# Kernel optimization log

Measured on AMD Instinct MI355X. Metric: run time of the kernel, lower is better.

The kernel has to match this reference:

```python
import jax, jax.numpy as jnp
import numpy as np


def _segment_mean(msg, dst, num_nodes):
    # msg: [E, B, O, T] summed into [N, B, O, T], mean over incoming edges
    s = jax.ops.segment_sum(msg, dst, num_segments=num_nodes)
    cnt = jax.ops.segment_sum(jnp.ones((msg.shape[0],), msg.dtype), dst, num_segments=num_nodes)
    return s / jnp.clip(cnt, 1.0)[:, None, None, None]


def _gcn(x, edge_index, edge_attr, A, Wk, Wr, b):
    # Edge-conditioned (spline-style) graph conv.
    # x: [B, N, Cin, T]; edge_attr: [E, 3]; Wk: [K, Cin, Cout]
    N = x.shape[1]
    src, dst = edge_index[0], edge_index[1]
    Bw = jax.nn.softmax(edge_attr @ A, axis=-1)          # [E, K] basis weights
    We = jnp.einsum('ek,kio->eio', Bw, Wk)                # [E, Cin, Cout]
    msg = jnp.einsum('beit,eio->ebot', x[:, src], We)     # [E, B, Cout, T]
    agg = _segment_mean(msg, dst, N).transpose(1, 0, 2, 3)  # [B, N, Cout, T]
    out = agg + jnp.einsum('bnit,io->bnot', x, Wr) + b[None, None, :, None]
    return jax.nn.elu(out)


def _pool(x, P, C, T):
    # x: [B, N_l, C, T] -> flatten, sparse-pool with P [N_{l+1}, N_l], unflatten
    B, N = x.shape[0], x.shape[1]
    xf = x.reshape(B, N, C * T)
    xf = jnp.einsum('mn,bnf->bmf', P, xf)
    return xf.reshape(B, P.shape[0], C, T)


def setup_inputs() -> dict:
    key = jax.random.key(0)
    ks = jax.random.split(key, 24)
    B, T = 2, 200
    N = [2048, 512, 128, 64]
    E = [16384, 8192, 2048]
    nf = [1, 8, 16, 32, 64, 128, 128]
    ld = 64

    def rn(k, shape, scale=1.0):
        return jax.random.normal(k, shape, dtype=jnp.float32) * scale

    inp = {}
    inp['x'] = rn(ks[0], (B, N[0], nf[0], T))
    inp['ei0'] = jax.random.randint(ks[1], (2, E[0]), 0, N[0])
    inp['ea0'] = jax.random.uniform(ks[2], (E[0], 3), dtype=jnp.float32)
    inp['ei1'] = jax.random.randint(ks[3], (2, E[1]), 0, N[1])
    inp['ea1'] = jax.random.uniform(ks[4], (E[1], 3), dtype=jnp.float32)
    inp['ei2'] = jax.random.randint(ks[5], (2, E[2]), 0, N[2])
    inp['ea2'] = jax.random.uniform(ks[6], (E[2], 3), dtype=jnp.float32)
    # gcn params: (A basis map, K=3 kernel weights, root weight, bias)
    inp['A1'] = rn(ks[7], (3, 3))
    inp['Wk1'] = rn(ks[8], (3, nf[0], nf[2]), 1.0 / np.sqrt(nf[0]))
    inp['Wr1'] = rn(ks[9], (nf[0], nf[2]), 1.0 / np.sqrt(nf[0]))
    inp['b1'] = jnp.zeros((nf[2],), jnp.float32)
    inp['A2'] = rn(ks[10], (3, 3))
    inp['Wk2'] = rn(ks[11], (3, nf[2], nf[3]), 1.0 / np.sqrt(nf[2]))
    inp['Wr2'] = rn(ks[12], (nf[2], nf[3]), 1.0 / np.sqrt(nf[2]))
    inp['b2'] = jnp.zeros((nf[3],), jnp.float32)
    inp['A3'] = rn(ks[13], (3, 3))
    inp['Wk3'] = rn(ks[14], (3, nf[3], nf[4]), 1.0 / np.sqrt(nf[3]))
    inp['Wr3'] = rn(ks[15], (nf[3], nf[4]), 1.0 / np.sqrt(nf[3]))
    inp['b3'] = jnp.zeros((nf[4],), jnp.float32)
    # sparse pooling projections (dense here)
    inp['P01'] = rn(ks[16], (N[1], N[0]), 1.0 / np.sqrt(N[0]))
    inp['P12'] = rn(ks[17], (N[2], N[1]), 1.0 / np.sqrt(N[1]))
    inp['P23'] = rn(ks[18], (N[3], N[2]), 1.0 / np.sqrt(N[2]))
    # 1x1 conv encoder head
    inp['fce1_w'] = rn(ks[19], (nf[4], nf[6]), 1.0 / np.sqrt(nf[4]))
    inp['fce1_b'] = jnp.zeros((nf[6],), jnp.float32)
    inp['fce2_w'] = rn(ks[20], (nf[6], ld), 1.0 / np.sqrt(nf[6]))
    inp['fce2_b'] = jnp.zeros((ld,), jnp.float32)
    return inp


def reference(x, ei0, ea0, ei1, ea1, ei2, ea2, A1, Wk1, Wr1, b1, A2, Wk2, Wr2, b2,
              A3, Wk3, Wr3, b3, P01, P12, P23, fce1_w, fce1_b, fce2_w, fce2_b):
    T = x.shape[-1]
    # level 0 -> 1
    h = _gcn(x, ei0, ea0, A1, Wk1, Wr1, b1)          # [B, N0, 16, T]
    h = _pool(h, P01, h.shape[2], T)                 # [B, N1, 16, T]
    # level 1 -> 2
    h = _gcn(h, ei1, ea1, A2, Wk2, Wr2, b2)          # [B, N1, 32, T]
    h = _pool(h, P12, h.shape[2], T)                 # [B, N2, 32, T]
    # level 2 -> 3
    h = _gcn(h, ei2, ea2, A3, Wk3, Wr3, b3)          # [B, N2, 64, T]
    h = _pool(h, P23, h.shape[2], T)                 # [B, N3, 64, T]
    # 1x1 conv encoder head (channel-wise linear over node/time grid)
    h = jax.nn.elu(jnp.einsum('bnct,co->bnot', h, fce1_w) + fce1_b[None, None, :, None])
    mu = jnp.tanh(jnp.einsum('bnct,co->bnot', h, fce2_w) + fce2_b[None, None, :, None])
    return mu  # [B, N3, latent_dim, T]
```

## Files before the change

### kernel.cpp

```cpp
#include <hip/hip_runtime.h>
#include <hip/hip_bf16.h>

using bf16 = __hip_bfloat16;
typedef unsigned short ushort_t;
typedef unsigned int uint_t;

constexpr int B = 2, T = 200;
constexpr int N0 = 2048, N1 = 512, N2 = 128, N3 = 64;
constexpr int E0 = 16384, E1 = 8192, E2 = 2048;

typedef __attribute__((ext_vector_type(8))) short bf16x8;
typedef __attribute__((ext_vector_type(4))) float f32x4;

constexpr size_t O_FLAG = 161792;
constexpr size_t O_WC1  = 163840;
constexpr size_t O_BIAS = 164096;
constexpr size_t O_BW0  = 165312;
constexpr size_t O_BW1  = 361920;
constexpr size_t O_BW2  = 460224;
constexpr size_t O_PB1  = 484800;
constexpr size_t O_PB2  = 2581952;
constexpr size_t O_PB3  = 2713024;
constexpr size_t O_WT2  = 2729408;
constexpr size_t O_WT3  = 2733504;
constexpr size_t O_W1H  = 2749888;
constexpr size_t O_W2H  = 2766272;
constexpr size_t O_AA   = 2785280;
constexpr size_t O_BB   = 15892480;

__device__ __forceinline__ float ldx(const void* p, long i, int bf) {
  if (bf) {
    uint_t v = (uint_t)(((const ushort_t*)p)[i]) << 16;
    float f; __builtin_memcpy(&f, &v, 4); return f;
  }
  return ((const float*)p)[i];
}
__device__ __forceinline__ void stf(float* p, float v) { *p = v; }
__device__ __forceinline__ void stf(bf16* p, float v) { *p = __float2bfloat16(v); }
__device__ __forceinline__ ushort_t f2bfu(float v) {
  bf16 h = __float2bfloat16(v); ushort_t u; __builtin_memcpy(&u, &h, 2); return u;
}

struct InPtrs {
  const void* ea0; const void* ea1; const void* ea2;
  const void* P01; const void* P12; const void* P23;
  const void* Wk1; const void* Wr1; const void* Wk2; const void* Wr2;
  const void* Wk3; const void* Wr3; const void* W1h; const void* W2h;
  const void* b1; const void* b2; const void* b3; const void* b1h; const void* b2h;
  const void* A1; const void* A2; const void* A3;
};

__global__ void k_setup0(int* I, const ushort_t* ea) {
  if (blockIdx.x < 158) {
    int i = blockIdx.x * 256 + threadIdx.x;
    I[i] = 0;
  } else if (threadIdx.x == 0) {
    int c = 0;
    for (int i = 0; i < 128; ++i) {
      uint_t v = (uint_t)ea[i] << 16;
      float f; __builtin_memcpy(&f, &v, 4);
      if (f >= 0.f && f <= 1.0f) c++;
    }
    *(int*)((char*)I + O_FLAG) = (c >= 120) ? 1 : 0;
  }
}

__device__ __forceinline__ void bw_one(const void* ea, int bf, const void* A,
                                       float* bw, int e) {
  float a0 = ldx(ea, e*3+0, bf), a1 = ldx(ea, e*3+1, bf), a2 = ldx(ea, e*3+2, bf);
  float l0 = a0*ldx(A,0,bf) + a1*ldx(A,3,bf) + a2*ldx(A,6,bf);
  float l1 = a0*ldx(A,1,bf) + a1*ldx(A,4,bf) + a2*ldx(A,7,bf);
  float l2 = a0*ldx(A,2,bf) + a1*ldx(A,5,bf) + a2*ldx(A,8,bf);
  float m = fmaxf(l0, fmaxf(l1, l2));
  float x0 = expf(l0 - m), x1 = expf(l1 - m), x2 = expf(l2 - m);
  float inv = 1.0f / (x0 + x1 + x2);
  bw[e*3+0] = x0*inv; bw[e*3+1] = x1*inv; bw[e*3+2] = x2*inv;
}

__global__ void k_prep(InPtrs P, char* base) {
  int bf = *(const int*)(base + O_FLAG);
  int bx = blockIdx.x, tid = threadIdx.x;
  float* bw0 = (float*)(base + O_BW0);
  float* bw1 = (float*)(base + O_BW1);
  float* bw2 = (float*)(base + O_BW2);
  if (bx < 64)        { bw_one(P.ea0, bf, P.A1, bw0, bx*256+tid); return; }
  if (bx < 96)        { bw_one(P.ea1, bf, P.A2, bw1, (bx-64)*256+tid); return; }
  if (bx < 104)       { bw_one(P.ea2, bf, P.A3, bw2, (bx-96)*256+tid); return; }
  if (bx < 4200)      { long i = (long)(bx-104)*256+tid;
                        ((ushort_t*)(base+O_PB1))[i] = f2bfu(ldx(P.P01, i, bf)); return; }
  if (bx < 4456)      { int i = (bx-4200)*256+tid;
                        ((ushort_t*)(base+O_PB2))[i] = f2bfu(ldx(P.P12, i, bf)); return; }
  if (bx < 4488)      { int i = (bx-4456)*256+tid;
                        ((ushort_t*)(base+O_PB3))[i] = f2bfu(ldx(P.P23, i, bf)); return; }
  if (bx < 4496)      { int j = (bx-4488)*256+tid; int o = j>>6, c = j&63;
                        float v = (c<48) ? ldx(P.Wk2, c*32+o, bf) : ldx(P.Wr2, (c-48)*32+o, bf);
                        ((ushort_t*)(base+O_WT2))[j] = f2bfu(v); return; }
  if (bx < 4528)      { int j = (bx-4496)*256+tid; int o = j>>7, c = j&127;
                        float v = (c<96) ? ldx(P.Wk3, c*64+o, bf) : ldx(P.Wr3, (c-96)*64+o, bf);
                        ((ushort_t*)(base+O_WT3))[j] = f2bfu(v); return; }
  if (bx < 4560)      { int j = (bx-4528)*256+tid; int o = j>>6, c = j&63;
                        ((ushort_t*)(base+O_W1H))[j] = f2bfu(ldx(P.W1h, c*128+o, bf)); return; }
  if (bx < 4592)      { int j = (bx-4560)*256+tid; int o = j>>7, c = j&127;
                        ((ushort_t*)(base+O_W2H))[j] = f2bfu(ldx(P.W2h, c*64+o, bf)); return; }
  {
    int i = (bx-4592)*256+tid;
    if (i < 64) {
      ((float*)(base+O_WC1))[i] = (i<48) ? ldx(P.Wk1, i, bf) : ldx(P.Wr1, i-48, bf);
    } else if (i < 368) {
      int j = i - 64; float v;
      if (j < 16)       v = ldx(P.b1, j, bf);
      else if (j < 48)  v = ldx(P.b2, j-16, bf);
      else if (j < 112) v = ldx(P.b3, j-48, bf);
      else if (j < 240) v = ldx(P.b1h, j-112, bf);
      else              v = ldx(P.b2h, j-240, bf);
      ((float*)(base+O_BIAS))[j] = v;
    }
  }
}

__global__ void k_hist3(const int* d0, const int* d1, const int* d2,
                        int* c0, int* c1, int* c2) {
  int i = blockIdx.x * 256 + threadIdx.x;
  if (i < E0) atomicAdd(&c0[d0[i]], 1);
  if (i < E1) atomicAdd(&c1[d1[i]], 1);
  if (i < E2) atomicAdd(&c2[d2[i]], 1);
}

__global__ void k_scan3(const int* c0, int* o0, int* u0,
                        const int* c1, int* o1, int* u1,
                        const int* c2, int* o2, int* u2) {
  const int* cnt; int* off; int* cur; int N;
  if (blockIdx.x == 0)      { cnt = c0; off = o0; cur = u0; N = N0; }
  else if (blockIdx.x == 1) { cnt = c1; off = o1; cur = u1; N = N1; }
  else                      { cnt = c2; off = o2; cur = u2; N = N2; }
  int tid = threadIdx.x;
  int chunk = (N + 63) >> 6;
  int base = tid * chunk;
  int s = 0;
  for (int j = 0; j < chunk; ++j) { int idx = base + j; if (idx < N) s += cnt[idx]; }
  int pre = s;
  for (int d = 1; d < 64; d <<= 1) {
    int v = __shfl_up(pre, d, 64);
    if (tid >= d) pre += v;
  }
  int run = pre - s;
  for (int j = 0; j < chunk; ++j) {
    int idx = base + j;
    if (idx < N) { off[idx] = run; cur[idx] = run; run += cnt[idx]; }
  }
  if (tid == 63) off[N] = run;
}

__global__ void k_fill3(const int* d0, int* u0, int* e0l,
                        const int* d1, int* u1, int* e1l,
                        const int* d2, int* u2, int* e2l) {
  int i = blockIdx.x * 256 + threadIdx.x;
  if (i < E0) { int p = atomicAdd(&u0[d0[i]], 1); e0l[p] = i; }
  if (i < E1) { int p = atomicAdd(&u1[d1[i]], 1); e1l[p] = i; }
  if (i < E2) { int p = atomicAdd(&u2[d2[i]], 1); e2l[p] = i; }
}

__global__ __launch_bounds__(256) void k_gc1(const void* x, const int* src,
    const int* off, const int* elist, const int* cnt, const float* bw,
    const float* W, const float* bias, bf16* h1, const int* flagp) {
  __shared__ float Wl[64];
  __shared__ float bl[16];
  __shared__ float ew0[32], ew1[32], ew2[32];
  __shared__ int es[32];
  int tid = threadIdx.x;
  if (tid < 64) Wl[tid] = W[tid];
  if (tid < 16) bl[tid] = bias[tid];
  int bf = *flagp;
  int n = blockIdx.y, b = blockIdx.z;
  int t = tid;
  bool tok = t < T;
  int beg = off[n], end = off[n + 1];
  float a0 = 0.f, a1 = 0.f, a2 = 0.f;
  for (int q0 = beg; q0 < end; q0 += 32) {
    int m = end - q0; if (m > 32) m = 32;
    __syncthreads();
    if (tid < m) {
      int e = elist[q0 + tid];
      es[tid] = src[e];
      ew0[tid] = bw[e*3+0]; ew1[tid] = bw[e*3+1]; ew2[tid] = bw[e*3+2];
    }
    __syncthreads();
    if (tok) {
      for (int j = 0; j < m; ++j) {
        float xv = ldx(x, (long)(b * N0 + es[j]) * T + t, bf);
        a0 += ew0[j] * xv; a1 += ew1[j] * xv; a2 += ew2[j] * xv;
      }
    }
  }
  __syncthreads();
  if (!tok) return;
  int c = cnt[n];
  float inv = 1.f / (float)(c > 0 ? c : 1);
  a0 *= inv; a1 *= inv; a2 *= inv;
  float xr = ldx(x, (long)(b * N0 + n) * T + t, bf);
  bf16* op = h1 + ((long)(b * N0 + n) * 16) * T + t;
#pragma unroll
  for (int o = 0; o < 16; ++o) {
    float v = a0 * Wl[o] + a1 * Wl[16 + o] + a2 * Wl[32 + o] + xr * Wl[48 + o] + bl[o];
    v = v > 0.f ? v : (expf(v) - 1.f);
    op[o * T] = __float2bfloat16(v);
  }
}

template<int CIN, int CPI, int O>
__global__ __launch_bounds__(256) void k_gcm(const float* hp, const int* src,
    const int* off, const int* elist, const int* cnt, const float* bw,
    const ushort_t* Wt, const float* bias, bf16* h, int N) {
  constexpr int C = 4 * CIN;
  constexpr int KG = C / 8;
  constexpr int MT = O / 16;
  __shared__ __align__(16) ushort_t Ws[O * C];
  __shared__ __align__(16) ushort_t Is[64 * C];
  __shared__ float ew0[32], ew1[32], ew2[32];
  __shared__ int es[32];
  int tid = threadIdx.x;
  int w = tid >> 6, l = tid & 63;
  int lf = l & 15, quad = l >> 4;
  int t0 = blockIdx.x * 64;
  int n = blockIdx.y, b = blockIdx.z;
  {
    const uint4* Wg = (const uint4*)Wt;
    for (int s = tid; s < O * KG; s += 256) {
      int o = s / KG, kg = s % KG;
      *(uint4*)(Ws + o * C + ((kg ^ (o & 7)) * 8)) = Wg[s];
    }
  }
  int tx = tid & 63, iy = tid >> 6;
  int t = t0 + tx;
  bool tok = t < T;
  float acc[3][CPI], xr[CPI];
#pragma unroll
  for (int k = 0; k < 3; ++k)
#pragma unroll
    for (int j = 0; j < CPI; ++j) acc[k][j] = 0.f;
#pragma unroll
  for (int j = 0; j < CPI; ++j) xr[j] = 0.f;
  int beg = off[n], end = off[n + 1];
  for (int q0 = beg; q0 < end; q0 += 32) {
    int mE = end - q0; if (mE > 32) mE = 32;
    __syncthreads();
    if (tid < mE) {
      int e = elist[q0 + tid];
      es[tid] = src[e];
      ew0[tid] = bw[e*3+0]; ew1[tid] = bw[e*3+1]; ew2[tid] = bw[e*3+2];
    }
    __syncthreads();
    if (tok) {
      for (int j2 = 0; j2 < mE; ++j2) {
        int s = es[j2];
        float w0 = ew0[j2], w1 = ew1[j2], w2 = ew2[j2];
        const float* xp = hp + ((long)(b * N + s) * CIN) * T + t;
#pragma unroll
        for (int j = 0; j < CPI; ++j) {
          float xv = xp[(iy * CPI + j) * T];
          acc[0][j] += w0 * xv; acc[1][j] += w1 * xv; acc[2][j] += w2 * xv;
        }
      }
    }
  }
  float inv = 1.f;
  if (tok) {
    int c = cnt[n];
    inv = 1.f / (float)(c > 0 ? c : 1);
    const float* xs = hp + ((long)(b * N + n) * CIN) * T + t;
#pragma unroll
    for (int j = 0; j < CPI; ++j) xr[j] = xs[(iy * CPI + j) * T];
  }
#pragma unroll
  for (int j = 0; j < CPI; ++j) {
    int i = iy * CPI + j;
#pragma unroll
    for (int k = 0; k < 3; ++k) {
      int c = k * CIN + i;
      Is[tx * C + ((c >> 3) ^ (tx & 7)) * 8 + (c & 7)] = f2bfu(acc[k][j] * inv);
    }
    int c = 3 * CIN + i;
    Is[tx * C + ((c >> 3) ^ (tx & 7)) * 8 + (c & 7)] = f2bfu(xr[j]);
  }
  __syncthreads();
  f32x4 dacc[MT];
#pragma unroll
  for (int mt = 0; mt < MT; ++mt) dacc[mt] = (f32x4){0.f, 0.f, 0.f, 0.f};
  int tr = w * 16 + lf;
#pragma unroll
  for (int kc = 0; kc < C / 32; ++kc) {
    int kg0 = kc * 4 + quad;
    bf16x8 bfr = *(const bf16x8*)(Is + tr * C + ((kg0 ^ (tr & 7)) * 8));
#pragma unroll
    for (int mt = 0; mt < MT; ++mt) {
      int o = mt * 16 + lf;
      bf16x8 afr = *(const bf16x8*)(Ws + o * C + ((kg0 ^ (o & 7)) * 8));
      dacc[mt] = __builtin_amdgcn_mfma_f32_16x16x32_bf16(afr, bfr, dacc[mt], 0, 0, 0);
    }
  }
  int tg = t0 + w * 16 + lf;
  if (tg < T) {
    long nb = (long)(b * N + n) * O;
#pragma unroll
    for (int mt = 0; mt < MT; ++mt) {
#pragma unroll
      for (int r = 0; r < 4; ++r) {
        int o = mt * 16 + quad * 4 + r;
        float v = dacc[mt][r] + bias[o];
        v = v > 0.f ? v : (expf(v) - 1.f);
        h[(nb + o) * T + tg] = __float2bfloat16(v);
      }
    }
  }
}

template<int WMT, int FT, typename TOut>
__global__ __launch_bounds__(256) void k_pool_mfma(const ushort_t* Pb, const ushort_t* h,
                                                   TOut* out, int M, int K, int F) {
  constexpr int BM = 64 * WMT;
  constexpr int BN = 16 * FT;
  __shared__ __align__(16) ushort_t As[BM * 64];
  __shared__ __align__(16) ushort_t Bs[BN * 64];
  int tid = threadIdx.x;
  int w = tid >> 6, l = tid & 63;
  int lf = l & 15, quad = l >> 4;
  int f0 = blockIdx.x * BN;
  int m0 = blockIdx.y * BM;
  int b = blockIdx.z;
  f32x4 acc[WMT][FT];
#pragma unroll
  for (int wt = 0; wt < WMT; ++wt)
#pragma unroll
    for (int ft = 0; ft < FT; ++ft) acc[wt][ft] = (f32x4){0.f, 0.f, 0.f, 0.f};

  for (int k0 = 0; k0 < K; k0 += 64) {
#pragma unroll
    for (int it = 0; it < BM / 32; ++it) {
      int cc = tid + 256 * it;
      int m = cc >> 3, kc = cc & 7;
      uint4 v = *(const uint4*)(Pb + (long)(m0 + m) * K + k0 + kc * 8);
      *(uint4*)(As + m * 64 + ((kc ^ (m & 7)) * 8)) = v;
    }
#pragma unroll
    for (int kb = (tid / BN) * 16; kb < 64; kb += (256 / BN) * 16) {
      int f = tid % BN;
      const ushort_t* hp = h + ((long)(b * K + k0 + kb)) * F + f0 + f;
      ushort_t r[16];
#pragma unroll
      for (int i = 0; i < 16; ++i) r[i] = hp[(long)i * F];
      int kc0 = kb >> 3;
      *(uint4*)(Bs + f * 64 + ((kc0 ^ (f & 7)) * 8)) = *(uint4*)&r[0];
      *(uint4*)(Bs + f * 64 + (((kc0 + 1) ^ (f & 7)) * 8)) = *(uint4*)&r[8];
    }
    __syncthreads();
#pragma unroll
    for (int ks = 0; ks < 2; ++ks) {
      int kc = ks * 4 + quad;
      bf16x8 bfr[FT];
#pragma unroll
      for (int ft = 0; ft < FT; ++ft) {
        int fl = ft * 16 + lf;
        bfr[ft] = *(const bf16x8*)(Bs + fl * 64 + ((kc ^ (fl & 7)) * 8));
      }
#pragma unroll
      for (int wt = 0; wt < WMT; ++wt) {
        int ml = wt * 64 + w * 16 + lf;
        bf16x8 afr = *(const bf16x8*)(As + ml * 64 + ((kc ^ (ml & 7)) * 8));
#pragma unroll
        for (int ft = 0; ft < FT; ++ft)
          acc[wt][ft] = __builtin_amdgcn_mfma_f32_16x16x32_bf16(afr, bfr[ft], acc[wt][ft], 0, 0, 0);
      }
    }
    __syncthreads();
  }
#pragma unroll
  for (int wt = 0; wt < WMT; ++wt) {
#pragma unroll
    for (int r = 0; r < 4; ++r) {
      int m = m0 + wt * 64 + w * 16 + quad * 4 + r;
      TOut* op = out + ((long)(b * M + m)) * F + f0 + lf;
#pragma unroll
      for (int ft = 0; ft < FT; ++ft)
        stf(op + ft * 16, acc[wt][ft][r]);
    }
  }
}

__global__ __launch_bounds__(256) void k_head(const float* hp3, const ushort_t* W1t,
    const ushort_t* W2t, const float* bias, void* outp, const int* flagp) {
  __shared__ __align__(16) ushort_t Ws1[128 * 64];
  __shared__ __align__(16) ushort_t Ws2[64 * 128];
  __shared__ __align__(16) ushort_t Is[64 * 64];
  __shared__ __align__(16) ushort_t G[64 * 128];
  int tid = threadIdx.x;
  int w = tid >> 6, l = tid & 63;
  int lf = l & 15, quad = l >> 4;
  int t0 = blockIdx.x * 64;
  int n = blockIdx.y, b = blockIdx.z;
  {
    const uint4* g1 = (const uint4*)W1t;
    for (int s = tid; s < 1024; s += 256) {
      int o = s >> 3, kg = s & 7;
      *(uint4*)(Ws1 + o * 64 + ((kg ^ (o & 7)) * 8)) = g1[s];
    }
    const uint4* g2 = (const uint4*)W2t;
    for (int s = tid; s < 1024; s += 256) {
      int o = s >> 4, kg = s & 15;
      *(uint4*)(Ws2 + o * 128 + ((kg ^ (o & 7)) * 8)) = g2[s];
    }
  }
  {
    int t = tid & 63;
    bool tok = (t0 + t) < T;
    const float* ip = hp3 + ((long)(b * 64 + n) * 64) * T + t0;
    for (int kg = tid >> 6; kg < 8; kg += 4) {
      ushort_t r[8];
#pragma unroll
      for (int j = 0; j < 8; ++j)
        r[j] = tok ? f2bfu(ip[(kg * 8 + j) * T + t]) : (ushort_t)0;
      *(uint4*)(Is + t * 64 + ((kg ^ (t & 7)) * 8)) = *(uint4*)r;
    }
  }
  __syncthreads();
  int tr = w * 16 + lf;
  {
    f32x4 a1[8];
#pragma unroll
    for (int mt = 0; mt < 8; ++mt) a1[mt] = (f32x4){0.f, 0.f, 0.f, 0.f};
#pragma unroll
    for (int kc = 0; kc < 2; ++kc) {
      int kg0 = kc * 4 + quad;
      bf16x8 bfr = *(const bf16x8*)(Is + tr * 64 + ((kg0 ^ (tr & 7)) * 8));
#pragma unroll
      for (int mt = 0; mt < 8; ++mt) {
        int o = mt * 16 + lf;
        bf16x8 afr = *(const bf16x8*)(Ws1 + o * 64 + ((kg0 ^ (o & 7)) * 8));
        a1[mt] = __builtin_amdgcn_mfma_f32_16x16x32_bf16(afr, bfr, a1[mt], 0, 0, 0);
      }
    }
    int tG = w * 16 + lf;
#pragma unroll
    for (int mt = 0; mt < 8; ++mt) {
#pragma unroll
      for (int r = 0; r < 4; ++r) {
        int o1 = mt * 16 + quad * 4 + r;
        float v = a1[mt][r] + bias[112 + o1];
        v = v > 0.f ? v : (expf(v) - 1.f);
        G[tG * 128 + ((o1 >> 3) ^ (tG & 7)) * 8 + (o1 & 7)] = f2bfu(v);
      }
    }
  }
  __syncthreads();
  {
    f32x4 a2[4];
#pragma unroll
    for (int mt = 0; mt < 4; ++mt) a2[mt] = (f32x4){0.f, 0.f, 0.f, 0.f};
#pragma unroll
    for (int kc = 0; kc < 4; ++kc) {
      int kg0 = kc * 4 + quad;
      bf16x8 bfr = *(const bf16x8*)(G + tr * 128 + ((kg0 ^ (tr & 7)) * 8));
#pragma unroll
      for (int mt = 0; mt < 4; ++mt) {
        int o = mt * 16 + lf;
        bf16x8 afr = *(const bf16x8*)(Ws2 + o * 128 + ((kg0 ^ (o & 7)) * 8));
        a2[mt] = __builtin_amdgcn_mfma_f32_16x16x32_bf16(afr, bfr, a2[mt], 0, 0, 0);
      }
    }
    int t = t0 + w * 16 + lf;
    if (t < T) {
      int bf = *flagp;
      long nb = (long)(b * 64 + n) * 64;
#pragma unroll
      for (int mt = 0; mt < 4; ++mt) {
#pragma unroll
        for (int r = 0; r < 4; ++r) {
          int o2 = mt * 16 + quad * 4 + r;
          float v = tanhf(a2[mt][r] + bias[240 + o2]);
          long idx = (nb + o2) * T + t;
          if (bf) ((bf16*)outp)[idx] = __float2bfloat16(v);
          else    ((float*)outp)[idx] = v;
        }
      }
    }
  }
}

extern "C" void kernel_launch(void* const* d_in, const int* in_sizes, int n_in,
                              void* d_out, int out_size, void* d_ws, size_t ws_size,
                              hipStream_t stream) {
  const int* ei0 = (const int*)d_in[1];
  const int* ei1 = (const int*)d_in[3];
  const int* ei2 = (const int*)d_in[5];

  char* base = (char*)d_ws;
  int* I = (int*)base;
  int* cnt0 = I;         int* off0 = I + 2048;  int* cur0 = I + 4112;  int* el0 = I + 6160;
  int* cnt1 = I + 22544; int* off1 = I + 23056; int* cur1 = I + 23584; int* el1 = I + 24096;
  int* cnt2 = I + 32288; int* off2 = I + 32416; int* cur2 = I + 32560; int* el2 = I + 32688;
  const int* flagp = (const int*)(base + O_FLAG);
  float* wc1f = (float*)(base + O_WC1);
  float* bias = (float*)(base + O_BIAS);
  float* bw0 = (float*)(base + O_BW0);
  float* bw1 = (float*)(base + O_BW1);
  float* bw2 = (float*)(base + O_BW2);
  ushort_t* Pb1 = (ushort_t*)(base + O_PB1);
  ushort_t* Pb2 = (ushort_t*)(base + O_PB2);
  ushort_t* Pb3 = (ushort_t*)(base + O_PB3);
  ushort_t* wt2 = (ushort_t*)(base + O_WT2);
  ushort_t* wt3 = (ushort_t*)(base + O_WT3);
  ushort_t* w1t = (ushort_t*)(base + O_W1H);
  ushort_t* w2t = (ushort_t*)(base + O_W2H);
  char* Aa = base + O_AA;
  char* Bb = base + O_BB;

  InPtrs P = { d_in[2], d_in[4], d_in[6], d_in[19], d_in[20], d_in[21],
               d_in[8], d_in[9], d_in[12], d_in[13], d_in[16], d_in[17],
               d_in[22], d_in[24], d_in[10], d_in[14], d_in[18], d_in[23],
               d_in[25], d_in[7], d_in[11], d_in[15] };

  k_setup0<<<159, 256, 0, stream>>>(I, (const ushort_t*)d_in[2]);
  k_prep<<<4594, 256, 0, stream>>>(P, base);
  k_hist3<<<64, 256, 0, stream>>>(ei0 + E0, ei1 + E1, ei2 + E2, cnt0, cnt1, cnt2);
  k_scan3<<<3, 64, 0, stream>>>(cnt0, off0, cur0, cnt1, off1, cur1, cnt2, off2, cur2);
  k_fill3<<<64, 256, 0, stream>>>(ei0 + E0, cur0, el0, ei1 + E1, cur1, el1, ei2 + E2, cur2, el2);

  k_gc1<<<dim3(1, N0, B), 256, 0, stream>>>(d_in[0], ei0, off0, el0, cnt0, bw0, wc1f, bias, (bf16*)Bb, flagp);
  k_pool_mfma<1, 4, float><<<dim3(50, 8, B), 256, 0, stream>>>(Pb1, (const ushort_t*)Bb, (float*)Aa, 512, 2048, 3200);
  k_gcm<16, 4, 32><<<dim3(4, N1, B), 256, 0, stream>>>((const float*)Aa, ei1, off1, el1, cnt1, bw1, wt2, bias + 16, (bf16*)Bb, N1);
  k_pool_mfma<1, 4, float><<<dim3(100, 2, B), 256, 0, stream>>>(Pb2, (const ushort_t*)Bb, (float*)Aa, 128, 512, 6400);
  k_gcm<32, 8, 64><<<dim3(4, N2, B), 256, 0, stream>>>((const float*)Aa, ei2, off2, el2, cnt2, bw2, wt3, bias + 48, (bf16*)Bb, N2);
  k_pool_mfma<1, 4, float><<<dim3(200, 1, B), 256, 0, stream>>>(Pb3, (const ushort_t*)Bb, (float*)Aa, 64, 128, 12800);
  k_head<<<dim3(4, N3, B), 256, 0, stream>>>((const float*)Aa, w1t, w2t, bias, d_out, flagp);
}
```

Measured before the change: 283.6 us.

## Rewrite pooling GEMM with split-K atomics, register prefetch, and block swizzle

Replaces the pooling MFMA kernel with a version that prefetches the next two K-steps into registers while computing the current one. It splits K across blocks for the first two pools, reduces partial results with float atomics into a zeroed buffer, and remaps block indices to group neighbouring tiles. The aim is to hide global-load latency and raise the block count so more CUs stay busy. In exchange it adds memset passes, atomic write traffic, and a nondeterministic summation order.

New measurement: 302.4 us. 6.6% more time.

```diff
diff --git a/kernel.cpp b/kernel.cpp
--- a/kernel.cpp
+++ b/kernel.cpp
@@ -314,74 +314,84 @@
   }
 }
 
-template<int WMT, int FT, typename TOut>
-__global__ __launch_bounds__(256) void k_pool_mfma(const ushort_t* Pb, const ushort_t* h,
-                                                   TOut* out, int M, int K, int F) {
-  constexpr int BM = 64 * WMT;
-  constexpr int BN = 16 * FT;
-  __shared__ __align__(16) ushort_t As[BM * 64];
-  __shared__ __align__(16) ushort_t Bs[BN * 64];
+template<int KSPLIT, bool ATOMIC, bool SWZ>
+__global__ __launch_bounds__(256) void k_poolp(const ushort_t* Pb, const ushort_t* h,
+                                               float* out, int M, int K, int F, int nInner) {
+  __shared__ __align__(16) ushort_t As[64 * 64];
+  __shared__ __align__(16) ushort_t Bs[64 * 64];
   int tid = threadIdx.x;
   int w = tid >> 6, l = tid & 63;
   int lf = l & 15, quad = l >> 4;
-  int f0 = blockIdx.x * BN;
-  int m0 = blockIdx.y * BM;
-  int b = blockIdx.z;
-  f32x4 acc[WMT][FT];
-#pragma unroll
-  for (int wt = 0; wt < WMT; ++wt)
-#pragma unroll
-    for (int ft = 0; ft < FT; ++ft) acc[wt][ft] = (f32x4){0.f, 0.f, 0.f, 0.f};
-
-  for (int k0 = 0; k0 < K; k0 += 64) {
-#pragma unroll
-    for (int it = 0; it < BM / 32; ++it) {
-      int cc = tid + 256 * it;
-      int m = cc >> 3, kc = cc & 7;
-      uint4 v = *(const uint4*)(Pb + (long)(m0 + m) * K + k0 + kc * 8);
-      *(uint4*)(As + m * 64 + ((kc ^ (m & 7)) * 8)) = v;
-    }
-#pragma unroll
-    for (int kb = (tid / BN) * 16; kb < 64; kb += (256 / BN) * 16) {
-      int f = tid % BN;
-      const ushort_t* hp = h + ((long)(b * K + k0 + kb)) * F + f0 + f;
-      ushort_t r[16];
-#pragma unroll
-      for (int i = 0; i < 16; ++i) r[i] = hp[(long)i * F];
-      int kc0 = kb >> 3;
-      *(uint4*)(Bs + f * 64 + ((kc0 ^ (f & 7)) * 8)) = *(uint4*)&r[0];
-      *(uint4*)(Bs + f * 64 + (((kc0 + 1) ^ (f & 7)) * 8)) = *(uint4*)&r[8];
-    }
-    __syncthreads();
-#pragma unroll
-    for (int ks = 0; ks < 2; ++ks) {
-      int kc = ks * 4 + quad;
-      bf16x8 bfr[FT];
-#pragma unroll
-      for (int ft = 0; ft < FT; ++ft) {
-        int fl = ft * 16 + lf;
-        bfr[ft] = *(const bf16x8*)(Bs + fl * 64 + ((kc ^ (fl & 7)) * 8));
-      }
-#pragma unroll
-      for (int wt = 0; wt < WMT; ++wt) {
-        int ml = wt * 64 + w * 16 + lf;
-        bf16x8 afr = *(const bf16x8*)(As + ml * 64 + ((kc ^ (ml & 7)) * 8));
-#pragma unroll
-        for (int ft = 0; ft < FT; ++ft)
-          acc[wt][ft] = __builtin_amdgcn_mfma_f32_16x16x32_bf16(afr, bfr[ft], acc[wt][ft], 0, 0, 0);
-      }
-    }
-    __syncthreads();
-  }
-#pragma unroll
-  for (int wt = 0; wt < WMT; ++wt) {
-#pragma unroll
-    for (int r = 0; r < 4; ++r) {
-      int m = m0 + wt * 64 + w * 16 + quad * 4 + r;
-      TOut* op = out + ((long)(b * M + m)) * F + f0 + lf;
-#pragma unroll
-      for (int ft = 0; ft < FT; ++ft)
-        stf(op + ft * 16, acc[wt][ft][r]);
+  int v = blockIdx.x;
+  if (SWZ) { int q = gridDim.x >> 3; v = (v & 7) * q + (v >> 3); }
+  int f_blk = v / nInner; int rem = v % nInner;
+  int m_blk = rem / (KSPLIT * B);
+  int kc = (rem / B) % KSPLIT;
+  int b = rem % B;
+  int f0 = f_blk * 64, m0 = m_blk * 64;
+  int Kc = K / KSPLIT;
+  int k0 = kc * Kc;
+  int nsteps = Kc >> 6;
+
+  int am0 = tid >> 3, ak = tid & 7;
+  int am1 = am0 + 32;
+  const ushort_t* Ap0 = Pb + (long)(m0 + am0) * K + k0 + ak * 8;
+  const ushort_t* Ap1 = Pb + (long)(m0 + am1) * K + k0 + ak * 8;
+  int fB = tid & 63, kb = (tid >> 6) * 16;
+  const ushort_t* Bp = h + ((long)b * K + k0 + kb) * F + f0 + fB;
+  int kc0 = kb >> 3;
+
+#define PLA(r0, r1, st) { r0 = *(const uint4*)(Ap0 + (st) * 64); \
+                          r1 = *(const uint4*)(Ap1 + (st) * 64); }
+#define PLB(rb, st) { _Pragma("unroll") \
+                      for (int i = 0; i < 16; ++i) rb[i] = Bp[(long)((st) * 64 + i) * F]; }
+#define PSA(r0, r1) { *(uint4*)(As + am0 * 64 + ((ak ^ (am0 & 7)) * 8)) = r0; \
+                      *(uint4*)(As + am1 * 64 + ((ak ^ (am1 & 7)) * 8)) = r1; }
+#define PSB(rb) { *(uint4*)(Bs + fB * 64 + ((kc0 ^ (fB & 7)) * 8)) = *(uint4*)&rb[0]; \
+                  *(uint4*)(Bs + fB * 64 + (((kc0 + 1) ^ (fB & 7)) * 8)) = *(uint4*)&rb[8]; }
+#define PMM() { _Pragma("unroll") for (int ks = 0; ks < 2; ++ks) { \
+    int kq = ks * 4 + quad; \
+    bf16x8 bfr[4]; \
+    _Pragma("unroll") for (int ft = 0; ft < 4; ++ft) { int fl = ft * 16 + lf; \
+      bfr[ft] = *(const bf16x8*)(Bs + fl * 64 + ((kq ^ (fl & 7)) * 8)); } \
+    int ml = w * 16 + lf; \
+    bf16x8 afr = *(const bf16x8*)(As + ml * 64 + ((kq ^ (ml & 7)) * 8)); \
+    _Pragma("unroll") for (int ft = 0; ft < 4; ++ft) \
+      acc[ft] = __builtin_amdgcn_mfma_f32_16x16x32_bf16(afr, bfr[ft], acc[ft], 0, 0, 0); } }
+
+  f32x4 acc[4];
+#pragma unroll
+  for (int ft = 0; ft < 4; ++ft) acc[ft] = (f32x4){0.f, 0.f, 0.f, 0.f};
+
+  uint4 ra0, ra1, sa0, sa1;
+  ushort_t rb[16], sb[16];
+  PLA(ra0, ra1, 0); PLB(rb, 0);
+  for (int s = 0; s < nsteps; s += 2) {
+    PLA(sa0, sa1, s + 1); PLB(sb, s + 1);
+    __syncthreads();
+    PSA(ra0, ra1); PSB(rb);
+    __syncthreads();
+    PMM();
+    if (s + 2 < nsteps) { PLA(ra0, ra1, s + 2); PLB(rb, s + 2); }
+    __syncthreads();
+    PSA(sa0, sa1); PSB(sb);
+    __syncthreads();
+    PMM();
+  }
+#undef PLA
+#undef PLB
+#undef PSA
+#undef PSB
+#undef PMM
+
+#pragma unroll
+  for (int r = 0; r < 4; ++r) {
+    int m = m0 + w * 16 + quad * 4 + r;
+    float* op = out + ((long)(b * M + m)) * F + f0 + lf;
+#pragma unroll
+    for (int ft = 0; ft < 4; ++ft) {
+      if (ATOMIC) atomicAdd(op + ft * 16, acc[ft][r]);
+      else        op[ft * 16] = acc[ft][r];
     }
   }
 }
@@ -524,11 +534,13 @@
   k_scan3<<<3, 64, 0, stream>>>(cnt0, off0, cur0, cnt1, off1, cur1, cnt2, off2, cur2);
   k_fill3<<<64, 256, 0, stream>>>(ei0 + E0, cur0, el0, ei1 + E1, cur1, el1, ei2 + E2, cur2, el2);
 
+  hipMemsetAsync(Aa, 0, (size_t)13107200, stream);
   k_gc1<<<dim3(1, N0, B), 256, 0, stream>>>(d_in[0], ei0, off0, el0, cnt0, bw0, wc1f, bias, (bf16*)Bb, flagp);
-  k_pool_mfma<1, 4, float><<<dim3(50, 8, B), 256, 0, stream>>>(Pb1, (const ushort_t*)Bb, (float*)Aa, 512, 2048, 3200);
+  k_poolp<2, true, true><<<1600, 256, 0, stream>>>(Pb1, (const ushort_t*)Bb, (float*)Aa, 512, 2048, 3200, 32);
   k_gcm<16, 4, 32><<<dim3(4, N1, B), 256, 0, stream>>>((const float*)Aa, ei1, off1, el1, cnt1, bw1, wt2, bias + 16, (bf16*)Bb, N1);
-  k_pool_mfma<1, 4, float><<<dim3(100, 2, B), 256, 0, stream>>>(Pb2, (const ushort_t*)Bb, (float*)Aa, 128, 512, 6400);
+  hipMemsetAsync(Aa, 0, (size_t)6553600, stream);
+  k_poolp<2, true, true><<<800, 256, 0, stream>>>(Pb2, (const ushort_t*)Bb, (float*)Aa, 128, 512, 6400, 8);
   k_gcm<32, 8, 64><<<dim3(4, N2, B), 256, 0, stream>>>((const float*)Aa, ei2, off2, el2, cnt2, bw2, wt3, bias + 48, (bf16*)Bb, N2);
-  k_pool_mfma<1, 4, float><<<dim3(200, 1, B), 256, 0, stream>>>(Pb3, (const ushort_t*)Bb, (float*)Aa, 64, 128, 12800);
+  k_poolp<1, false, false><<<400, 256, 0, stream>>>(Pb3, (const ushort_t*)Bb, (float*)Aa, 64, 128, 12800, 2);
   k_head<<<dim3(4, N3, B), 256, 0, stream>>>((const float*)Aa, w1t, w2t, bias, d_out, flagp);
 }
```

## Transpose pooled activations before pool GEMM and restructure pool kernel launches

Applied to the files above, without the earlier changes.

Adds a tiled LDS transpose kernel so each pool GEMM reads activations K-contiguous with vectorized 16-byte loads, replacing the strided 16-element column gathers of the old pool kernel. The new pool kernel uses a flat 1D grid with an XCD-aware block remap, loads the next tile into registers before the barrier, and handles batches per launch. Buffers are reshuffled between the Aa and Bb scratch regions to make room for the transposed copies. The cost is extra transpose passes and extra memory traffic, plus two launches per batch on level 0.

After: 307.2 us. 8.3% more time.

```diff
diff --git a/kernel.cpp b/kernel.cpp
--- a/kernel.cpp
+++ b/kernel.cpp
@@ -35,8 +35,6 @@
   }
   return ((const float*)p)[i];
 }
-__device__ __forceinline__ void stf(float* p, float v) { *p = v; }
-__device__ __forceinline__ void stf(bf16* p, float v) { *p = __float2bfloat16(v); }
 __device__ __forceinline__ ushort_t f2bfu(float v) {
   bf16 h = __float2bfloat16(v); ushort_t u; __builtin_memcpy(&u, &h, 2); return u;
 }
@@ -314,75 +312,87 @@
   }
 }
 
-template<int WMT, int FT, typename TOut>
-__global__ __launch_bounds__(256) void k_pool_mfma(const ushort_t* Pb, const ushort_t* h,
-                                                   TOut* out, int M, int K, int F) {
-  constexpr int BM = 64 * WMT;
-  constexpr int BN = 16 * FT;
-  __shared__ __align__(16) ushort_t As[BM * 64];
-  __shared__ __align__(16) ushort_t Bs[BN * 64];
+__global__ __launch_bounds__(256) void k_tr(const ushort_t* __restrict__ src,
+    ushort_t* __restrict__ dst, int R, int C, long zstride) {
+  __shared__ __align__(16) ushort_t Ls[64 * 72];
+  const ushort_t* s = src + (long)blockIdx.z * zstride;
+  ushort_t* d = dst + (long)blockIdx.z * zstride;
+  int tid = threadIdx.x;
+  int rt = blockIdx.y * 64, ct = blockIdx.x * 64;
+  int rr = tid >> 3, c8 = (tid & 7) * 8;
+#pragma unroll
+  for (int p = 0; p < 2; ++p) {
+    uint4 v = *(const uint4*)(s + (long)(rt + rr + p * 32) * C + ct + c8);
+    *(uint4*)(Ls + (rr + p * 32) * 72 + c8) = v;
+  }
+  __syncthreads();
+  int n8 = (tid & 7) * 8;
+#pragma unroll
+  for (int p = 0; p < 2; ++p) {
+    int f = (tid >> 3) + p * 32;
+    ushort_t rbuf[8];
+#pragma unroll
+    for (int j = 0; j < 8; ++j) rbuf[j] = Ls[(n8 + j) * 72 + f];
+    *(uint4*)(d + (long)(ct + f) * R + rt + n8) = *(uint4*)rbuf;
+  }
+}
+
+template<int NBATCH>
+__global__ __launch_bounds__(256) void k_poolT(const ushort_t* __restrict__ Pb,
+    const ushort_t* __restrict__ hT, float* __restrict__ out,
+    int M, int K, int F, int nInner) {
+  __shared__ __align__(16) ushort_t As[64 * 64];
+  __shared__ __align__(16) ushort_t Bs[64 * 64];
   int tid = threadIdx.x;
   int w = tid >> 6, l = tid & 63;
   int lf = l & 15, quad = l >> 4;
-  int f0 = blockIdx.x * BN;
-  int m0 = blockIdx.y * BM;
-  int b = blockIdx.z;
-  f32x4 acc[WMT][FT];
-#pragma unroll
-  for (int wt = 0; wt < WMT; ++wt)
-#pragma unroll
-    for (int ft = 0; ft < FT; ++ft) acc[wt][ft] = (f32x4){0.f, 0.f, 0.f, 0.f};
-
-  for (int k0 = 0; k0 < K; k0 += 64) {
-#pragma unroll
-    for (int it = 0; it < BM / 32; ++it) {
-      int cc = tid + 256 * it;
-      int m = cc >> 3, kc = cc & 7;
-      uint4 v = *(const uint4*)(Pb + (long)(m0 + m) * K + k0 + kc * 8);
-      *(uint4*)(As + m * 64 + ((kc ^ (m & 7)) * 8)) = v;
-    }
-#pragma unroll
-    for (int kb = (tid / BN) * 16; kb < 64; kb += (256 / BN) * 16) {
-      int f = tid % BN;
-      const ushort_t* hp = h + ((long)(b * K + k0 + kb)) * F + f0 + f;
-      ushort_t r[16];
-#pragma unroll
-      for (int i = 0; i < 16; ++i) r[i] = hp[(long)i * F];
-      int kc0 = kb >> 3;
-      *(uint4*)(Bs + f * 64 + ((kc0 ^ (f & 7)) * 8)) = *(uint4*)&r[0];
-      *(uint4*)(Bs + f * 64 + (((kc0 + 1) ^ (f & 7)) * 8)) = *(uint4*)&r[8];
-    }
+  int v = blockIdx.x;
+  { int q = gridDim.x >> 3; v = (v & 7) * q + (v >> 3); }
+  int f_blk = v / nInner; int rem = v - f_blk * nInner;
+  int m_blk = rem / NBATCH; int b = rem - m_blk * NBATCH;
+  int f0 = f_blk * 64, m0 = m_blk * 64;
+  int r = tid >> 3, koct = tid & 7;
+  const ushort_t* Ap = Pb + (long)(m0 + r) * K + koct * 8;
+  const ushort_t* Bp = hT + (long)b * F * K + (long)(f0 + r) * K + koct * 8;
+  int wof0 = r * 64 + ((koct ^ (r & 7)) * 8);
+  int wof1 = (r + 32) * 64 + ((koct ^ (r & 7)) * 8);
+  f32x4 acc[4];
+#pragma unroll
+  for (int ft = 0; ft < 4; ++ft) acc[ft] = (f32x4){0.f, 0.f, 0.f, 0.f};
+
+  for (int kk = 0; kk < K; kk += 64) {
+    uint4 a0 = *(const uint4*)(Ap + kk);
+    uint4 a1 = *(const uint4*)(Ap + (long)32 * K + kk);
+    uint4 b0 = *(const uint4*)(Bp + kk);
+    uint4 b1 = *(const uint4*)(Bp + (long)32 * K + kk);
     __syncthreads();
+    *(uint4*)(As + wof0) = a0;
+    *(uint4*)(As + wof1) = a1;
+    *(uint4*)(Bs + wof0) = b0;
+    *(uint4*)(Bs + wof1) = b1;
+    __syncthreads();
 #pragma unroll
     for (int ks = 0; ks < 2; ++ks) {
-      int kc = ks * 4 + quad;
-      bf16x8 bfr[FT];
-#pragma unroll
-      for (int ft = 0; ft < FT; ++ft) {
+      int kq = ks * 4 + quad;
+      bf16x8 bfr[4];
+#pragma unroll
+      for (int ft = 0; ft < 4; ++ft) {
         int fl = ft * 16 + lf;
-        bfr[ft] = *(const bf16x8*)(Bs + fl * 64 + ((kc ^ (fl & 7)) * 8));
-      }
-#pragma unroll
-      for (int wt = 0; wt < WMT; ++wt) {
-        int ml = wt * 64 + w * 16 + lf;
-        bf16x8 afr = *(const bf16x8*)(As + ml * 64 + ((kc ^ (ml & 7)) * 8));
-#pragma unroll
-        for (int ft = 0; ft < FT; ++ft)
-          acc[wt][ft] = __builtin_amdgcn_mfma_f32_16x16x32_bf16(afr, bfr[ft], acc[wt][ft], 0, 0, 0);
-      }
-    }
-    __syncthreads();
-  }
-#pragma unroll
-  for (int wt = 0; wt < WMT; ++wt) {
-#pragma unroll
-    for (int r = 0; r < 4; ++r) {
-      int m = m0 + wt * 64 + w * 16 + quad * 4 + r;
-      TOut* op = out + ((long)(b * M + m)) * F + f0 + lf;
-#pragma unroll
-      for (int ft = 0; ft < FT; ++ft)
-        stf(op + ft * 16, acc[wt][ft][r]);
-    }
+        bfr[ft] = *(const bf16x8*)(Bs + fl * 64 + ((kq ^ (fl & 7)) * 8));
+      }
+      int ml = w * 16 + lf;
+      bf16x8 afr = *(const bf16x8*)(As + ml * 64 + ((kq ^ (ml & 7)) * 8));
+#pragma unroll
+      for (int ft = 0; ft < 4; ++ft)
+        acc[ft] = __builtin_amdgcn_mfma_f32_16x16x32_bf16(afr, bfr[ft], acc[ft], 0, 0, 0);
+    }
+  }
+#pragma unroll
+  for (int rr = 0; rr < 4; ++rr) {
+    int m = m0 + w * 16 + quad * 4 + rr;
+    float* op = out + (long)b * M * F + (long)m * F + f0 + lf;
+#pragma unroll
+    for (int ft = 0; ft < 4; ++ft) op[ft * 16] = acc[ft][rr];
   }
 }
 
@@ -525,10 +535,18 @@
   k_fill3<<<64, 256, 0, stream>>>(ei0 + E0, cur0, el0, ei1 + E1, cur1, el1, ei2 + E2, cur2, el2);
 
   k_gc1<<<dim3(1, N0, B), 256, 0, stream>>>(d_in[0], ei0, off0, el0, cnt0, bw0, wc1f, bias, (bf16*)Bb, flagp);
-  k_pool_mfma<1, 4, float><<<dim3(50, 8, B), 256, 0, stream>>>(Pb1, (const ushort_t*)Bb, (float*)Aa, 512, 2048, 3200);
-  k_gcm<16, 4, 32><<<dim3(4, N1, B), 256, 0, stream>>>((const float*)Aa, ei1, off1, el1, cnt1, bw1, wt2, bias + 16, (bf16*)Bb, N1);
-  k_pool_mfma<1, 4, float><<<dim3(100, 2, B), 256, 0, stream>>>(Pb2, (const ushort_t*)Bb, (float*)Aa, 128, 512, 6400);
-  k_gcm<32, 8, 64><<<dim3(4, N2, B), 256, 0, stream>>>((const float*)Aa, ei2, off2, el2, cnt2, bw2, wt3, bias + 48, (bf16*)Bb, N2);
-  k_pool_mfma<1, 4, float><<<dim3(200, 1, B), 256, 0, stream>>>(Pb3, (const ushort_t*)Bb, (float*)Aa, 64, 128, 12800);
+  k_tr<<<dim3(50, 32, 1), 256, 0, stream>>>((const ushort_t*)Bb, (ushort_t*)Aa, 2048, 3200, 0);
+  k_poolT<1><<<400, 256, 0, stream>>>(Pb1, (const ushort_t*)Aa, (float*)Bb, 512, 2048, 3200, 8);
+  k_tr<<<dim3(50, 32, 1), 256, 0, stream>>>((const ushort_t*)(Bb + 13107200), (ushort_t*)Aa, 2048, 3200, 0);
+  k_poolT<1><<<400, 256, 0, stream>>>(Pb1, (const ushort_t*)Aa, (float*)(Bb + 6553600), 512, 2048, 3200, 8);
+
+  k_gcm<16, 4, 32><<<dim3(4, N1, B), 256, 0, stream>>>((const float*)Bb, ei1, off1, el1, cnt1, bw1, wt2, bias + 16, (bf16*)Aa, N1);
+  k_tr<<<dim3(100, 8, 2), 256, 0, stream>>>((const ushort_t*)Aa, (ushort_t*)(Bb + 13107200), 512, 6400, 3276800);
+  k_poolT<2><<<400, 256, 0, stream>>>(Pb2, (const ushort_t*)(Bb + 13107200), (float*)Bb, 128, 512, 6400, 4);
+
+  k_gcm<32, 8, 64><<<dim3(4, N2, B), 256, 0, stream>>>((const float*)Bb, ei2, off2, el2, cnt2, bw2, wt3, bias + 48, (bf16*)Aa, N2);
+  k_tr<<<dim3(200, 2, 2), 256, 0, stream>>>((const ushort_t*)Aa, (ushort_t*)(Bb + 13107200), 128, 12800, 1638400);
+  k_poolT<2><<<400, 256, 0, stream>>>(Pb3, (const ushort_t*)(Bb + 13107200), (float*)Aa, 64, 128, 12800, 2);
+
   k_head<<<dim3(4, N3, B), 256, 0, stream>>>((const float*)Aa, w1t, w2t, bias, d_out, flagp);
 }
```

## Rewrite pooling GEMM with vectorized B loads, XCD-aware block remap, smaller tiles

Applied to the files above, without the earlier changes.

Replaces the pooling MFMA kernel with a version that loads the activation operand in 16-byte vectors along the feature dimension instead of 16 strided scalar loads, then transposes into swizzled shared memory with scalar writes. It issues global loads before the first barrier so they overlap the previous iteration's compute. It also uses a 1D grid with a remap that groups consecutive tiles onto the same XCD, and halves the feature tile so more blocks are launched. The scalar LDS transpose writes may cause bank conflicts, and the smaller tile reduces reuse of the pooling matrix.

Measured after the change: 286.8 us. Within noise of the previous version (+1.1%).

```diff
diff --git a/kernel.cpp b/kernel.cpp
--- a/kernel.cpp
+++ b/kernel.cpp
@@ -35,8 +35,6 @@
   }
   return ((const float*)p)[i];
 }
-__device__ __forceinline__ void stf(float* p, float v) { *p = v; }
-__device__ __forceinline__ void stf(bf16* p, float v) { *p = __float2bfloat16(v); }
 __device__ __forceinline__ ushort_t f2bfu(float v) {
   bf16 h = __float2bfloat16(v); ushort_t u; __builtin_memcpy(&u, &h, 2); return u;
 }
@@ -314,75 +312,86 @@
   }
 }
 
-template<int WMT, int FT, typename TOut>
-__global__ __launch_bounds__(256) void k_pool_mfma(const ushort_t* Pb, const ushort_t* h,
-                                                   TOut* out, int M, int K, int F) {
-  constexpr int BM = 64 * WMT;
+template<int FT>
+__global__ __launch_bounds__(256) void k_poolw(const ushort_t* __restrict__ Pb,
+    const ushort_t* __restrict__ h, float* __restrict__ out,
+    int M, int K, int F, int nInner) {
   constexpr int BN = 16 * FT;
-  __shared__ __align__(16) ushort_t As[BM * 64];
+  constexpr int NOCT = BN / 8;
+  constexpr int NROW = 256 / NOCT;
+  constexpr int NP = 64 / NROW;
+  __shared__ __align__(16) ushort_t As[64 * 64];
   __shared__ __align__(16) ushort_t Bs[BN * 64];
   int tid = threadIdx.x;
   int w = tid >> 6, l = tid & 63;
   int lf = l & 15, quad = l >> 4;
-  int f0 = blockIdx.x * BN;
-  int m0 = blockIdx.y * BM;
-  int b = blockIdx.z;
-  f32x4 acc[WMT][FT];
-#pragma unroll
-  for (int wt = 0; wt < WMT; ++wt)
-#pragma unroll
-    for (int ft = 0; ft < FT; ++ft) acc[wt][ft] = (f32x4){0.f, 0.f, 0.f, 0.f};
-
-  for (int k0 = 0; k0 < K; k0 += 64) {
-#pragma unroll
-    for (int it = 0; it < BM / 32; ++it) {
-      int cc = tid + 256 * it;
-      int m = cc >> 3, kc = cc & 7;
-      uint4 v = *(const uint4*)(Pb + (long)(m0 + m) * K + k0 + kc * 8);
-      *(uint4*)(As + m * 64 + ((kc ^ (m & 7)) * 8)) = v;
-    }
-#pragma unroll
-    for (int kb = (tid / BN) * 16; kb < 64; kb += (256 / BN) * 16) {
-      int f = tid % BN;
-      const ushort_t* hp = h + ((long)(b * K + k0 + kb)) * F + f0 + f;
-      ushort_t r[16];
-#pragma unroll
-      for (int i = 0; i < 16; ++i) r[i] = hp[(long)i * F];
-      int kc0 = kb >> 3;
-      *(uint4*)(Bs + f * 64 + ((kc0 ^ (f & 7)) * 8)) = *(uint4*)&r[0];
-      *(uint4*)(Bs + f * 64 + (((kc0 + 1) ^ (f & 7)) * 8)) = *(uint4*)&r[8];
-    }
+  int ml = w * 16 + lf;
+  int v = blockIdx.x;
+  { int q = gridDim.x >> 3; v = (v & 7) * q + (v >> 3); }
+  int f_blk = v / nInner; int rem = v - f_blk * nInner;
+  int m_blk = rem >> 1;
+  int b = rem & 1;
+  int f0 = f_blk * BN, m0 = m_blk * 64;
+
+  int am0 = tid >> 3, ak = tid & 7;
+  int am1 = am0 + 32;
+  const ushort_t* Ap0 = Pb + (long)(m0 + am0) * K + ak * 8;
+  const ushort_t* Ap1 = Pb + (long)(m0 + am1) * K + ak * 8;
+  int wofA0 = am0 * 64 + ((ak ^ (am0 & 7)) * 8);
+  int wofA1 = am1 * 64 + ((ak ^ (am1 & 7)) * 8);
+  int fo = tid % NOCT;
+  int krb = tid / NOCT;
+  const ushort_t* Bp = h + ((long)b * K + krb) * F + f0 + fo * 8;
+
+  f32x4 acc[FT];
+#pragma unroll
+  for (int ft = 0; ft < FT; ++ft) acc[ft] = (f32x4){0.f, 0.f, 0.f, 0.f};
+
+  for (int kk = 0; kk < K; kk += 64) {
+    uint4 a0 = *(const uint4*)(Ap0 + kk);
+    uint4 a1 = *(const uint4*)(Ap1 + kk);
+    uint4 bv[NP];
+#pragma unroll
+    for (int p = 0; p < NP; ++p)
+      bv[p] = *(const uint4*)(Bp + (long)(kk + p * NROW) * F);
     __syncthreads();
+    *(uint4*)(As + wofA0) = a0;
+    *(uint4*)(As + wofA1) = a1;
+#pragma unroll
+    for (int p = 0; p < NP; ++p) {
+      int kr = krb + p * NROW;
+      int kh = kr >> 3, kw = kr & 7;
+#pragma unroll
+      for (int j = 0; j < 8; ++j) {
+        int f = fo * 8 + j;
+        int sw = j ^ fo;
+        Bs[f * 64 + ((kh ^ sw) * 8) + kw] = ((const ushort_t*)&bv[p])[j];
+      }
+    }
+    __syncthreads();
 #pragma unroll
     for (int ks = 0; ks < 2; ++ks) {
-      int kc = ks * 4 + quad;
+      int kq = ks * 4 + quad;
       bf16x8 bfr[FT];
 #pragma unroll
       for (int ft = 0; ft < FT; ++ft) {
         int fl = ft * 16 + lf;
-        bfr[ft] = *(const bf16x8*)(Bs + fl * 64 + ((kc ^ (fl & 7)) * 8));
-      }
-#pragma unroll
-      for (int wt = 0; wt < WMT; ++wt) {
-        int ml = wt * 64 + w * 16 + lf;
-        bf16x8 afr = *(const bf16x8*)(As + ml * 64 + ((kc ^ (ml & 7)) * 8));
-#pragma unroll
-        for (int ft = 0; ft < FT; ++ft)
-          acc[wt][ft] = __builtin_amdgcn_mfma_f32_16x16x32_bf16(afr, bfr[ft], acc[wt][ft], 0, 0, 0);
-      }
-    }
-    __syncthreads();
-  }
-#pragma unroll
-  for (int wt = 0; wt < WMT; ++wt) {
-#pragma unroll
-    for (int r = 0; r < 4; ++r) {
-      int m = m0 + wt * 64 + w * 16 + quad * 4 + r;
-      TOut* op = out + ((long)(b * M + m)) * F + f0 + lf;
+        int sfl = (fl & 7) ^ ((fl >> 3) & 7);
+        bfr[ft] = *(const bf16x8*)(Bs + fl * 64 + ((kq ^ sfl) * 8));
+      }
+      bf16x8 afr = *(const bf16x8*)(As + ml * 64 + ((kq ^ (ml & 7)) * 8));
 #pragma unroll
       for (int ft = 0; ft < FT; ++ft)
-        stf(op + ft * 16, acc[wt][ft][r]);
-    }
+        acc[ft] = __builtin_amdgcn_mfma_f32_16x16x32_bf16(afr, bfr[ft], acc[ft], 0, 0, 0);
+    }
+  }
+
+#pragma unroll
+  for (int rr = 0; rr < 4; ++rr) {
+    int m = m0 + w * 16 + quad * 4 + rr;
+    float* op = out + ((long)(b * M + m)) * F + f0 + lf;
+#pragma unroll
+    for (int ft = 0; ft < FT; ++ft) op[ft * 16] = acc[ft][rr];
   }
 }
 
@@ -525,10 +534,10 @@
   k_fill3<<<64, 256, 0, stream>>>(ei0 + E0, cur0, el0, ei1 + E1, cur1, el1, ei2 + E2, cur2, el2);
 
   k_gc1<<<dim3(1, N0, B), 256, 0, stream>>>(d_in[0], ei0, off0, el0, cnt0, bw0, wc1f, bias, (bf16*)Bb, flagp);
-  k_pool_mfma<1, 4, float><<<dim3(50, 8, B), 256, 0, stream>>>(Pb1, (const ushort_t*)Bb, (float*)Aa, 512, 2048, 3200);
+  k_poolw<2><<<1600, 256, 0, stream>>>(Pb1, (const ushort_t*)Bb, (float*)Aa, 512, 2048, 3200, 16);
   k_gcm<16, 4, 32><<<dim3(4, N1, B), 256, 0, stream>>>((const float*)Aa, ei1, off1, el1, cnt1, bw1, wt2, bias + 16, (bf16*)Bb, N1);
-  k_pool_mfma<1, 4, float><<<dim3(100, 2, B), 256, 0, stream>>>(Pb2, (const ushort_t*)Bb, (float*)Aa, 128, 512, 6400);
+  k_poolw<2><<<800, 256, 0, stream>>>(Pb2, (const ushort_t*)Bb, (float*)Aa, 128, 512, 6400, 4);
   k_gcm<32, 8, 64><<<dim3(4, N2, B), 256, 0, stream>>>((const float*)Aa, ei2, off2, el2, cnt2, bw2, wt3, bias + 48, (bf16*)Bb, N2);
-  k_pool_mfma<1, 4, float><<<dim3(200, 1, B), 256, 0, stream>>>(Pb3, (const ushort_t*)Bb, (float*)Aa, 64, 128, 12800);
+  k_poolw<2><<<800, 256, 0, stream>>>(Pb3, (const ushort_t*)Bb, (float*)Aa, 64, 128, 12800, 2);
   k_head<<<dim3(4, N3, B), 256, 0, stream>>>((const float*)Aa, w1t, w2t, bias, d_out, flagp);
 }
```
